# Optimization experiments

Measured on AMD Instinct MI355X. Metric: run time of the kernel, lower is better.

## Reference

```python
import jax, jax.numpy as jnp
import numpy as np
from jax import lax

B, C, O, H, W = 4, 96, 96, 128, 128
K = 3      # kernel size everywhere
D = 2      # dilation of dconv
KK = K * K


def conv2d(x, w, b, pad, dil=1):
    # x: [B,C,H,W], w: [O,C,K,K]
    y = lax.conv_general_dilated(
        x, w, window_strides=(1, 1), padding=[(pad, pad), (pad, pad)],
        rhs_dilation=(dil, dil), dimension_numbers=('NCHW', 'OIHW', 'NCHW'))
    return y + b[None, :, None, None]


def bilinear_sample(img, py, px):
    # img: [B,C,H,W]; py,px: [B,KK,H,W] float sample coords (zero outside)
    y0 = jnp.floor(py)
    x0 = jnp.floor(px)
    wy = py - y0
    wx = px - x0
    flat = img.reshape(B, 1, C, H * W)  # broadcast over KK

    def gather(yi, xi):
        valid = (yi >= 0) & (yi < H) & (xi >= 0) & (xi < W)
        yc = jnp.clip(yi, 0, H - 1).astype(jnp.int32)
        xc = jnp.clip(xi, 0, W - 1).astype(jnp.int32)
        idx = (yc * W + xc).reshape(B, KK, 1, H * W)
        g = jnp.take_along_axis(flat, idx, axis=3)  # [B,KK,C,H*W]
        g = g.reshape(B, KK, C, H, W)
        return g * valid.reshape(B, KK, 1, H, W)

    v00 = gather(y0, x0)
    v01 = gather(y0, x0 + 1)
    v10 = gather(y0 + 1, x0)
    v11 = gather(y0 + 1, x0 + 1)
    wy = wy[:, :, None]
    wx = wx[:, :, None]
    return ((1 - wy) * ((1 - wx) * v00 + wx * v01)
            + wy * ((1 - wx) * v10 + wx * v11))


def setup_inputs() -> dict:
    key = jax.random.key(0)
    ks = jax.random.split(key, 7)
    x = jax.random.normal(ks[0], (B, C, H, W), jnp.float32)
    s = 1.0 / np.sqrt(C * K * K)  # torch default conv init bound
    u = lambda k, shape: jax.random.uniform(k, shape, jnp.float32, -s, s)
    return dict(
        x=x,
        dconv_w=u(ks[1], (O, C, K, K)), dconv_b=u(ks[2], (O,)),
        off_w=u(ks[3], (2 * KK, C, K, K)), off_b=u(ks[4], (2 * KK,)),
        def_w=u(ks[5], (O, C, K, K)), def_b=u(ks[6], (O,)),
    )


def reference(x, dconv_w, dconv_b, off_w, off_b, def_w, def_b):
    # dilated conv + relu + residual (self.conv is unused in the original forward)
    x1 = conv2d(x, dconv_w, dconv_b, pad=D, dil=D)
    x3 = x + jax.nn.relu(x1)

    # offset prediction: [B, 2*KK, H, W] -> (dy, dx) per kernel tap
    offset = conv2d(x3, off_w, off_b, pad=1)
    off = offset.reshape(B, KK, 2, H, W)
    dy, dx = off[:, :, 0], off[:, :, 1]

    # base sampling grid: output pixel + kernel tap - padding
    ki, kj = jnp.meshgrid(jnp.arange(K), jnp.arange(K), indexing='ij')
    ky = (ki.reshape(-1) - (K - 1) // 2).astype(jnp.float32)  # [KK]
    kx = (kj.reshape(-1) - (K - 1) // 2).astype(jnp.float32)
    ygrid = jnp.arange(H, dtype=jnp.float32)[:, None]
    xgrid = jnp.arange(W, dtype=jnp.float32)[None, :]
    py = ygrid[None, None] + ky[None, :, None, None] + dy  # [B,KK,H,W]
    px = xgrid[None, None] + kx[None, :, None, None] + dx

    sampled = bilinear_sample(x3, py, px)  # [B,KK,C,H,W]
    out = jnp.einsum('bkchw,ock->bohw', sampled, def_w.reshape(O, C, KK))
    return out + def_b[None, :, None, None]
```

## Files before the change

### kernel.cpp

```cpp
#include <hip/hip_runtime.h>
#include <hip/hip_bf16.h>

#define BD 4
#define CD 96
#define OD 96
#define HD 128
#define WD 128
#define HWD (HD*WD)
#define PLANEB ((size_t)(BD*HWD)*64)

typedef __attribute__((ext_vector_type(8))) short bfrag;
typedef __attribute__((ext_vector_type(4))) float ffrag;

__device__ __forceinline__ short f2bs(float f) {
    __hip_bfloat16 h = __float2bfloat16(f);
    return *reinterpret_cast<short*>(&h);
}

__device__ __forceinline__ bfrag interp4(bfrag c00, bfrag c01, bfrag c10, bfrag c11,
                                         float f00, float f01, float f10, float f11) {
    const int* i00 = (const int*)&c00;
    const int* i01 = (const int*)&c01;
    const int* i10 = (const int*)&c10;
    const int* i11 = (const int*)&c11;
    int ap[4];
    #pragma unroll
    for (int d = 0; d < 4; d++) {
        float a0 = __int_as_float(((unsigned)i00[d]) << 16);
        float b0 = __int_as_float(((unsigned)i01[d]) << 16);
        float c0 = __int_as_float(((unsigned)i10[d]) << 16);
        float d0 = __int_as_float(((unsigned)i11[d]) << 16);
        float a1 = __int_as_float(i00[d] & 0xffff0000);
        float b1 = __int_as_float(i01[d] & 0xffff0000);
        float c1 = __int_as_float(i10[d] & 0xffff0000);
        float d1 = __int_as_float(i11[d] & 0xffff0000);
        float rlo = f00*a0 + f01*b0 + f10*c0 + f11*d0;
        float rhi = f00*a1 + f01*b1 + f10*c1 + f11*d1;
        ap[d] = (int)((unsigned short)f2bs(rlo)) |
                ((int)((unsigned short)f2bs(rhi)) << 16);
    }
    return *(const bfrag*)ap;
}

__device__ __forceinline__ int swizzle512(int gid) {
    return ((gid & 7) << 6) | (gid >> 3);
}

__global__ __launch_bounds__(256) void k_transpose(const float* __restrict__ x,
                                                   char* __restrict__ xbP) {
    __shared__ short tile[64 * 104];
    int pix0 = blockIdx.x * 64;
    int b = pix0 / HWD; int hw0 = pix0 % HWD;
    int tid = threadIdx.x;

    for (int e = tid; e < 96*16; e += 256) {
        int c = e >> 4, g = e & 15;
        float4 v = *(const float4*)(x + ((size_t)(b*96 + c))*HWD + hw0 + 4*g);
        tile[(4*g+0)*104 + c] = f2bs(v.x);
        tile[(4*g+1)*104 + c] = f2bs(v.y);
        tile[(4*g+2)*104 + c] = f2bs(v.z);
        tile[(4*g+3)*104 + c] = f2bs(v.w);
    }
    __syncthreads();
    for (int e = tid; e < 64*12; e += 256) {
        int px = e / 12, c8 = e % 12;
        int sc = c8 >> 2, ck = c8 & 3;
        bfrag v = *(const bfrag*)(tile + px*104 + c8*8);
        *(bfrag*)(xbP + (size_t)sc*PLANEB + ((size_t)(pix0 + px))*64 + ck*16) = v;
    }
}

__global__ void k_repack(const float* __restrict__ dconv_w,
                         const float* __restrict__ off_w,
                         const float* __restrict__ def_w,
                         short* __restrict__ wB1,
                         short* __restrict__ wB2,
                         short* __restrict__ wB) {
    int t = blockIdx.x * blockDim.x + threadIdx.x;
    if (t < 27648) {
        int j = t & 7; int l = (t >> 3) & 63; int tile = t >> 9;
        int s = tile >> 1, nt = tile & 1;
        int k = 32*s + (l >> 4)*8 + j;
        int o = 16*nt + (l & 15);
        int c = k % 96, tap = k / 96;
        wB2[t] = (o < 18) ? f2bs(off_w[(o*96 + c)*9 + tap]) : (short)0;
    }
    if (t < 82944) {
        int j = t & 7; int l = (t >> 3) & 63; int tile = t >> 9;
        int s = tile / 6, nt = tile % 6;
        int k = 32*s + (l >> 4)*8 + j;
        int o = 16*nt + (l & 15);
        int c = k % 96, tap = k / 96;
        wB1[t] = f2bs(dconv_w[(o*96 + c)*9 + tap]);
        wB[t]  = f2bs(def_w [(o*96 + c)*9 + tap]);
    }
}

#define SLICE_SHORTS 9216

__global__ __launch_bounds__(512, 2) void k_conv1(const float* __restrict__ x,
                                                  const char* __restrict__ xbP,
                                                  const short* __restrict__ wB,
                                                  const float* __restrict__ bias,
                                                  char* __restrict__ x3P) {
    __shared__ short wbuf[2][SLICE_SHORTS];

    int pix0 = swizzle512(blockIdx.x) * 128;
    int b = pix0 / HWD; int hw0 = pix0 % HWD;
    int h = hw0 / WD;
    int tid = threadIdx.x;
    int l = tid & 63, wv = tid >> 6;
    int q = l >> 4, mr = l & 15;
    int px0w = 16*wv;
    const bfrag az = {0,0,0,0,0,0,0,0};

    {
        bfrag s0, s1, s2;
        int c2 = tid + 1024;
        s0 = *(const bfrag*)(wB + tid*8);
        s1 = *(const bfrag*)(wB + (tid+512)*8);
        if (c2 < 1152) s2 = *(const bfrag*)(wB + c2*8);
        *(bfrag*)&wbuf[0][tid*8]       = s0;
        *(bfrag*)&wbuf[0][(tid+512)*8] = s1;
        if (c2 < 1152) *(bfrag*)&wbuf[0][c2*8] = s2;
    }
    __syncthreads();

    ffrag acc[6];
    #pragma unroll
    for (int nt = 0; nt < 6; nt++) acc[nt] = ffrag{0.f,0.f,0.f,0.f};

    int cur = 0;
    #pragma unroll 1
    for (int tap = 0; tap < 9; tap++) {
        bfrag s0, s1, s2;
        if (tap < 8) {
            const short* src = wB + (size_t)(tap+1)*SLICE_SHORTS;
            int c2 = tid + 1024;
            s0 = *(const bfrag*)(src + tid*8);
            s1 = *(const bfrag*)(src + (tid+512)*8);
            if (c2 < 1152) s2 = *(const bfrag*)(src + c2*8);
        }

        int y = h + (tap/3)*2 - 2;
        int yc = min(max(y, 0), HD-1);
        int xx = px0w + mr + (tap%3)*2 - 2;
        int xxc = min(max(xx, 0), WD-1);
        bool v = ((unsigned)y < HD) && ((unsigned)xx < WD);
        size_t u = ((size_t)(b*HWD + yc*WD + xxc))*64 + q*16;
        #pragma unroll
        for (int sc = 0; sc < 3; sc++) {
            bfrag a = *(const bfrag*)(xbP + (size_t)sc*PLANEB + u);
            if (!v) a = az;
            const short* wp = &wbuf[cur][(sc*6)*512 + l*8];
            #pragma unroll
            for (int nt = 0; nt < 6; nt++) {
                bfrag bb = *(const bfrag*)(wp + nt*512);
                acc[nt] = __builtin_amdgcn_mfma_f32_16x16x32_bf16(a, bb, acc[nt], 0, 0, 0);
            }
        }

        if (tap < 8) {
            int c2 = tid + 1024;
            *(bfrag*)&wbuf[cur^1][tid*8]       = s0;
            *(bfrag*)&wbuf[cur^1][(tid+512)*8] = s1;
            if (c2 < 1152) *(bfrag*)&wbuf[cur^1][c2*8] = s2;
        }
        __syncthreads();
        cur ^= 1;
    }

    short (*etile)[104] = (short(*)[104])&wbuf[0][0];
    {
        int lrow = px0w + q*4;
        int hwb = hw0 + lrow;
        #pragma unroll
        for (int nt = 0; nt < 6; nt++) {
            int o = 16*nt + mr;
            float bo = bias[o];
            float4 xr = *(const float4*)(x + ((size_t)(b*96 + o))*HWD + hwb);
            etile[lrow+0][o] = f2bs(xr.x + fmaxf(acc[nt][0] + bo, 0.f));
            etile[lrow+1][o] = f2bs(xr.y + fmaxf(acc[nt][1] + bo, 0.f));
            etile[lrow+2][o] = f2bs(xr.z + fmaxf(acc[nt][2] + bo, 0.f));
            etile[lrow+3][o] = f2bs(xr.w + fmaxf(acc[nt][3] + bo, 0.f));
        }
    }
    __syncthreads();
    for (int e = tid; e < 128*12; e += 512) {
        int px = e / 12, c8 = e % 12;
        int sc = c8 >> 2, ck = c8 & 3;
        bfrag v = *(const bfrag*)&etile[px][c8*8];
        *(bfrag*)(x3P + (size_t)sc*PLANEB + ((size_t)(b*HWD + hw0 + px))*64 + ck*16) = v;
    }
}

__global__ __launch_bounds__(512, 2) void k_deform(const char* __restrict__ x3P,
                                                   const short* __restrict__ wB2,
                                                   const float* __restrict__ off_b,
                                                   const short* __restrict__ wB,
                                                   const float* __restrict__ def_b,
                                                   float* __restrict__ out) {
    __shared__ __align__(16) char smem[36864 + 12288];
    short (*wbuf)[SLICE_SHORTS] = (short(*)[SLICE_SHORTS])smem;
    short* cb = (short*)(smem + 36864);
    float (*offsb)[20] = (float(*)[20])(smem + 36864);

    int pix0 = swizzle512(blockIdx.x) * 128;
    int b = pix0 / HWD; int hw0 = pix0 % HWD;
    int h = hw0 / WD;
    int tid = threadIdx.x;
    int l = tid & 63, wv = tid >> 6;
    int q = l >> 4, mr = l & 15;
    int px0w = 16*wv;
    const bfrag az = {0,0,0,0,0,0,0,0};

    {
        bfrag s0, s1, s2;
        int c2 = tid + 1024;
        s0 = *(const bfrag*)(wB + tid*8);
        s1 = *(const bfrag*)(wB + (tid+512)*8);
        if (c2 < 1152) s2 = *(const bfrag*)(wB + c2*8);
        *(bfrag*)&wbuf[0][tid*8]       = s0;
        *(bfrag*)&wbuf[0][(tid+512)*8] = s1;
        if (c2 < 1152) *(bfrag*)&wbuf[0][c2*8] = s2;
        if (tid < 384) {
            bfrag sc2 = *(const bfrag*)(wB2 + tid*8);
            *(bfrag*)&cb[tid*8] = sc2;
        }
    }
    __syncthreads();

    ffrag oa0 = ffrag{0.f,0.f,0.f,0.f};
    ffrag oa1 = ffrag{0.f,0.f,0.f,0.f};

    int c2cur = 0;
    #pragma unroll 1
    for (int tap = 0; tap < 9; tap++) {
        bfrag sn;
        bool act = (tid < 384) && (tap < 8);
        if (act) sn = *(const bfrag*)(wB2 + (size_t)(tap+1)*3072 + tid*8);

        int y = h + tap/3 - 1;
        int yc = min(max(y, 0), HD-1);
        int xx = px0w + mr + tap%3 - 1;
        int xxc = min(max(xx, 0), WD-1);
        bool v = ((unsigned)y < HD) && ((unsigned)xx < WD);
        size_t u = ((size_t)(b*HWD + yc*WD + xxc))*64 + q*16;
        #pragma unroll
        for (int sc = 0; sc < 3; sc++) {
            const short* wb = cb + c2cur*3072 + (sc*2)*512 + l*8;
            bfrag b0 = *(const bfrag*)(wb);
            bfrag b1 = *(const bfrag*)(wb + 512);
            bfrag a = *(const bfrag*)(x3P + (size_t)sc*PLANEB + u);
            if (!v) a = az;
            oa0 = __builtin_amdgcn_mfma_f32_16x16x32_bf16(a, b0, oa0, 0, 0, 0);
            oa1 = __builtin_amdgcn_mfma_f32_16x16x32_bf16(a, b1, oa1, 0, 0, 0);
        }

        if (act) *(bfrag*)&cb[(c2cur^1)*3072 + tid*8] = sn;
        __syncthreads();
        c2cur ^= 1;
    }

    {
        int row = px0w + q*4;
        float bo0 = off_b[mr];
        #pragma unroll
        for (int r = 0; r < 4; r++) offsb[row + r][mr] = oa0[r] + bo0;
        if (mr < 2) {
            float bo1 = off_b[16 + mr];
            #pragma unroll
            for (int r = 0; r < 4; r++) offsb[row + r][16 + mr] = oa1[r] + bo1;
        }
    }

    ffrag acc[6];
    #pragma unroll
    for (int nt = 0; nt < 6; nt++) acc[nt] = ffrag{0.f,0.f,0.f,0.f};

    int cur = 0;
    #pragma unroll 1
    for (int tap = 0; tap < 9; tap++) {
        bfrag s0, s1, s2;
        if (tap < 8) {
            const short* src = wB + (size_t)(tap+1)*SLICE_SHORTS;
            int c2 = tid + 1024;
            s0 = *(const bfrag*)(src + tid*8);
            s1 = *(const bfrag*)(src + (tid+512)*8);
            if (c2 < 1152) s2 = *(const bfrag*)(src + c2*8);
        }

        size_t po[4];
        float fbv[4];
        {
            int lp = px0w + mr;
            float dy = offsb[lp][2*tap];
            float dx = offsb[lp][2*tap + 1];
            float py  = (float)(h  + tap/3 - 1) + dy;
            float pxf = (float)(lp + tap%3 - 1) + dx;
            float y0f = floorf(py), x0f = floorf(pxf);
            float wy = py - y0f, wx = pxf - x0f;
            int y0 = (int)y0f, x0 = (int)x0f;
            int y1 = y0 + 1, x1 = x0 + 1;
            bool vy0 = (unsigned)y0 < HD, vy1 = (unsigned)y1 < HD;
            bool vx0 = (unsigned)x0 < WD, vx1 = (unsigned)x1 < WD;
            fbv[0] = (vy0 && vx0) ? (1.f-wy)*(1.f-wx) : 0.f;
            fbv[1] = (vy0 && vx1) ? (1.f-wy)*wx       : 0.f;
            fbv[2] = (vy1 && vx0) ? wy*(1.f-wx)       : 0.f;
            fbv[3] = (vy1 && vx1) ? wy*wx             : 0.f;
            int yc0 = min(max(y0,0),HD-1), yc1 = min(max(y1,0),HD-1);
            int xc0 = min(max(x0,0),WD-1), xc1 = min(max(x1,0),WD-1);
            po[0] = ((size_t)(b*HWD + yc0*WD + xc0))*64 + q*16;
            po[1] = ((size_t)(b*HWD + yc0*WD + xc1))*64 + q*16;
            po[2] = ((size_t)(b*HWD + yc1*WD + xc0))*64 + q*16;
            po[3] = ((size_t)(b*HWD + yc1*WD + xc1))*64 + q*16;
        }
        #pragma unroll
        for (int sc = 0; sc < 3; sc++) {
            const char* pb = x3P + (size_t)sc*PLANEB;
            const short* wp = &wbuf[cur][(sc*6)*512 + l*8];
            bfrag bbf[6];
            #pragma unroll
            for (int nt = 0; nt < 6; nt++) bbf[nt] = *(const bfrag*)(wp + nt*512);
            bfrag c00 = *(const bfrag*)(pb + po[0]);
            bfrag c01 = *(const bfrag*)(pb + po[1]);
            bfrag c10 = *(const bfrag*)(pb + po[2]);
            bfrag c11 = *(const bfrag*)(pb + po[3]);
            bfrag a = interp4(c00, c01, c10, c11, fbv[0], fbv[1], fbv[2], fbv[3]);
            #pragma unroll
            for (int nt = 0; nt < 6; nt++)
                acc[nt] = __builtin_amdgcn_mfma_f32_16x16x32_bf16(a, bbf[nt], acc[nt], 0, 0, 0);
        }

        if (tap < 8) {
            int c2 = tid + 1024;
            *(bfrag*)&wbuf[cur^1][tid*8]       = s0;
            *(bfrag*)&wbuf[cur^1][(tid+512)*8] = s1;
            if (c2 < 1152) *(bfrag*)&wbuf[cur^1][c2*8] = s2;
        }
        __syncthreads();
        cur ^= 1;
    }

    int hwb = hw0 + px0w + q*4;
    #pragma unroll
    for (int nt = 0; nt < 6; nt++) {
        int o = 16*nt + mr;
        float bo = def_b[o];
        float4 v;
        v.x = acc[nt][0] + bo; v.y = acc[nt][1] + bo;
        v.z = acc[nt][2] + bo; v.w = acc[nt][3] + bo;
        *(float4*)(out + ((size_t)(b*96 + o))*HWD + hwb) = v;
    }
}

extern "C" void kernel_launch(void* const* d_in, const int* in_sizes, int n_in,
                              void* d_out, int out_size, void* d_ws, size_t ws_size,
                              hipStream_t stream) {
    const float* x       = (const float*)d_in[0];
    const float* dconv_w = (const float*)d_in[1];
    const float* dconv_b = (const float*)d_in[2];
    const float* off_w   = (const float*)d_in[3];
    const float* off_b   = (const float*)d_in[4];
    const float* def_w   = (const float*)d_in[5];
    const float* def_b   = (const float*)d_in[6];
    float* out = (float*)d_out;

    char* ws = (char*)d_ws;
    char*  xbP  = ws;
    char*  x3P  = ws + 12582912;
    short* wB1  = (short*)(ws + 25165824);
    short* wB2  = (short*)(ws + 25331712);
    short* wB   = (short*)(ws + 25387008);

    k_repack<<<324, 256, 0, stream>>>(dconv_w, off_w, def_w, wB1, wB2, wB);
    k_transpose<<<(BD*HWD)/64, 256, 0, stream>>>(x, xbP);
    k_conv1<<<(BD*HWD)/128, 512, 0, stream>>>(x, xbP, wB1, dconv_b, x3P);
    k_deform<<<(BD*HWD)/128, 512, 0, stream>>>(x3P, wB2, off_b, wB, def_b, out);
}
```

Baseline: 156.6 us.

## Prefetch next tap's bilinear corners and use barrier without vmem drain

Computes the sampling coordinates and weights for the next tap one iteration ahead and issues the four corner gathers for channel plane 0 early, so gather latency overlaps the current tap's MFMAs. It replaces __syncthreads with a barrier that waits only on LDS counters, leaving the in-flight global loads outstanding across the barrier. Byte offsets are narrowed from size_t to 32-bit unsigned. This costs extra registers for the prefetched fragments, which may lower occupancy.

```diff
diff --git a/kernel.cpp b/kernel.cpp
--- a/kernel.cpp
+++ b/kernel.cpp
@@ -15,6 +15,11 @@
 __device__ __forceinline__ short f2bs(float f) {
     __hip_bfloat16 h = __float2bfloat16(f);
     return *reinterpret_cast<short*>(&h);
+}
+
+__device__ __forceinline__ void barrier_nodrain() {
+    asm volatile("s_waitcnt lgkmcnt(0)" ::: "memory");
+    __builtin_amdgcn_s_barrier();
 }
 
 __device__ __forceinline__ bfrag interp4(bfrag c00, bfrag c01, bfrag c10, bfrag c11,
@@ -278,6 +283,36 @@
     #pragma unroll
     for (int nt = 0; nt < 6; nt++) acc[nt] = ffrag{0.f,0.f,0.f,0.f};
 
+    auto prep = [&](int tap, unsigned (&po)[4], float (&fbv)[4]) {
+        int lp = px0w + mr;
+        float dy = offsb[lp][2*tap];
+        float dx = offsb[lp][2*tap + 1];
+        float py  = (float)(h  + tap/3 - 1) + dy;
+        float pxf = (float)(lp + tap%3 - 1) + dx;
+        float y0f = floorf(py), x0f = floorf(pxf);
+        float wy = py - y0f, wx = pxf - x0f;
+        int y0 = (int)y0f, x0 = (int)x0f;
+        int y1 = y0 + 1, x1 = x0 + 1;
+        bool vy0 = (unsigned)y0 < HD, vy1 = (unsigned)y1 < HD;
+        bool vx0 = (unsigned)x0 < WD, vx1 = (unsigned)x1 < WD;
+        fbv[0] = (vy0 && vx0) ? (1.f-wy)*(1.f-wx) : 0.f;
+        fbv[1] = (vy0 && vx1) ? (1.f-wy)*wx       : 0.f;
+        fbv[2] = (vy1 && vx0) ? wy*(1.f-wx)       : 0.f;
+        fbv[3] = (vy1 && vx1) ? wy*wx             : 0.f;
+        int yc0 = min(max(y0,0),HD-1), yc1 = min(max(y1,0),HD-1);
+        int xc0 = min(max(x0,0),WD-1), xc1 = min(max(x1,0),WD-1);
+        po[0] = (unsigned)((b*HWD + yc0*WD + xc0)*64 + q*16);
+        po[1] = (unsigned)((b*HWD + yc0*WD + xc1)*64 + q*16);
+        po[2] = (unsigned)((b*HWD + yc1*WD + xc0)*64 + q*16);
+        po[3] = (unsigned)((b*HWD + yc1*WD + xc1)*64 + q*16);
+    };
+
+    unsigned po[4]; float fbv[4];
+    prep(0, po, fbv);
+    bfrag p0[4];
+    #pragma unroll
+    for (int k = 0; k < 4; k++) p0[k] = *(const bfrag*)(x3P + po[k]);
+
     int cur = 0;
     #pragma unroll 1
     for (int tap = 0; tap < 9; tap++) {
@@ -289,34 +324,25 @@
             s1 = *(const bfrag*)(src + (tid+512)*8);
             if (c2 < 1152) s2 = *(const bfrag*)(src + c2*8);
         }
-
-        size_t po[4];
-        float fbv[4];
+        unsigned pon[4]; float fbn[4]; bfrag pn0[4];
+        if (tap < 8) {
+            prep(tap+1, pon, fbn);
+            #pragma unroll
+            for (int k = 0; k < 4; k++) pn0[k] = *(const bfrag*)(x3P + pon[k]);
+        }
         {
-            int lp = px0w + mr;
-            float dy = offsb[lp][2*tap];
-            float dx = offsb[lp][2*tap + 1];
-            float py  = (float)(h  + tap/3 - 1) + dy;
-            float pxf = (float)(lp + tap%3 - 1) + dx;
-            float y0f = floorf(py), x0f = floorf(pxf);
-            float wy = py - y0f, wx = pxf - x0f;
-            int y0 = (int)y0f, x0 = (int)x0f;
-            int y1 = y0 + 1, x1 = x0 + 1;
-            bool vy0 = (unsigned)y0 < HD, vy1 = (unsigned)y1 < HD;
-            bool vx0 = (unsigned)x0 < WD, vx1 = (unsigned)x1 < WD;
-            fbv[0] = (vy0 && vx0) ? (1.f-wy)*(1.f-wx) : 0.f;
-            fbv[1] = (vy0 && vx1) ? (1.f-wy)*wx       : 0.f;
-            fbv[2] = (vy1 && vx0) ? wy*(1.f-wx)       : 0.f;
-            fbv[3] = (vy1 && vx1) ? wy*wx             : 0.f;
-            int yc0 = min(max(y0,0),HD-1), yc1 = min(max(y1,0),HD-1);
-            int xc0 = min(max(x0,0),WD-1), xc1 = min(max(x1,0),WD-1);
-            po[0] = ((size_t)(b*HWD + yc0*WD + xc0))*64 + q*16;
-            po[1] = ((size_t)(b*HWD + yc0*WD + xc1))*64 + q*16;
-            po[2] = ((size_t)(b*HWD + yc1*WD + xc0))*64 + q*16;
-            po[3] = ((size_t)(b*HWD + yc1*WD + xc1))*64 + q*16;
+            const short* wp = &wbuf[cur][0*512 + l*8];
+            bfrag bbf[6];
+            #pragma unroll
+            for (int nt = 0; nt < 6; nt++) bbf[nt] = *(const bfrag*)(wp + nt*512);
+            bfrag a = interp4(p0[0], p0[1], p0[2], p0[3],
+                              fbv[0], fbv[1], fbv[2], fbv[3]);
+            #pragma unroll
+            for (int nt = 0; nt < 6; nt++)
+                acc[nt] = __builtin_amdgcn_mfma_f32_16x16x32_bf16(a, bbf[nt], acc[nt], 0, 0, 0);
         }
         #pragma unroll
-        for (int sc = 0; sc < 3; sc++) {
+        for (int sc = 1; sc < 3; sc++) {
             const char* pb = x3P + (size_t)sc*PLANEB;
             const short* wp = &wbuf[cur][(sc*6)*512 + l*8];
             bfrag bbf[6];
@@ -331,14 +357,19 @@
             for (int nt = 0; nt < 6; nt++)
                 acc[nt] = __builtin_amdgcn_mfma_f32_16x16x32_bf16(a, bbf[nt], acc[nt], 0, 0, 0);
         }
-
         if (tap < 8) {
             int c2 = tid + 1024;
             *(bfrag*)&wbuf[cur^1][tid*8]       = s0;
             *(bfrag*)&wbuf[cur^1][(tid+512)*8] = s1;
             if (c2 < 1152) *(bfrag*)&wbuf[cur^1][c2*8] = s2;
         }
-        __syncthreads();
+        barrier_nodrain();
+        if (tap < 8) {
+            #pragma unroll
+            for (int k = 0; k < 4; k++) {
+                po[k] = pon[k]; fbv[k] = fbn[k]; p0[k] = pn0[k];
+            }
+        }
         cur ^= 1;
     }
 
```

Measured after the change: 171.6 us. +9.6%, slower.
